# Kernel tuning notes

Hardware: AMD Instinct MI355X
Metric: run time of the kernel (lower is better)

Reference implementation:

```python
import jax, jax.numpy as jnp
import numpy as np

LOW_T = 0.3
HIGH_T = 0.7
H_IMG = 2048
W_IMG = 2048


def _any8(a, g):
    # OR over the 8 neighbors at offset +-g (the original connected() checks
    # the 8 compass neighbors at distance `gap`).
    H, W = a.shape
    p = jnp.pad(a, g)
    def s(dy, dx):
        return p[g + dy:g + dy + H, g + dx:g + dx + W]
    return (s(-g, -g) | s(-g, 0) | s(-g, g)
            | s(0, -g) | s(0, g)
            | s(g, -g) | s(g, 0) | s(g, g))


def _bound_mask(H, W, g):
    # original boundary rule: x-g >= 0, y-g >= 0, x+g < W-1, y+g < H-1
    y = jnp.arange(H)[:, None]
    x = jnp.arange(W)[None, :]
    return (x >= g) & (y >= g) & (x + g < W - 1) & (y + g < H - 1)


def _hysteresis_active(lt2, hi2):
    # Fixed point of the flood-fill: weak pixels (low>0) become active when
    # 8-connected (gap 1 or 2) to an active pixel. Parallel conditional
    # dilation iterated to convergence.
    H, W = lt2.shape
    tmask = _bound_mask(H, W, 1)   # trace() in-bounds condition
    c1 = _bound_mask(H, W, 1)
    c2 = _bound_mask(H, W, 2)
    weak = lt2 > 0.0

    def cond(state):
        return state[1]

    def body(state):
        active, _ = state
        conn = (c1 & _any8(active, 1)) | (c2 & _any8(active, 2))
        new = active | (tmask & weak & conn)
        return new, jnp.any(new != active)

    active0 = hi2 > 0.0
    active, _ = jax.lax.while_loop(cond, body, (active0, jnp.array(True)))
    return active


def setup_inputs() -> dict:
    key = jax.random.key(0)
    k1, k2, k3 = jax.random.split(key, 3)
    shape = (1, 1, H_IMG, W_IMG)
    return {
        "thin_edges": jax.random.uniform(k1, shape, jnp.float32),
        "grad_magnitude": jax.random.normal(k2, shape, jnp.float32),
        "grad_orientation": jax.random.normal(k3, shape, jnp.float32),
    }


def reference(thin_edges, grad_magnitude, grad_orientation):
    low_thresholded = jnp.where(thin_edges < LOW_T, 0.0, thin_edges)
    high_threshold = jnp.where(thin_edges < HIGH_T, 0.0, thin_edges)
    lt2 = low_thresholded[0, 0]
    hi2 = high_threshold[0, 0]
    active = _hysteresis_active(lt2, hi2)
    # strong pixels keep their (high) value; promoted weak pixels take low value
    final2 = jnp.where(hi2 > 0.0, hi2, jnp.where(active, lt2, 0.0))
    final_thresholded = final2[None, None]
    return (low_thresholded, high_threshold, final_thresholded)
```

## Files before the change

### kernel.cpp

```cpp
#include <hip/hip_runtime.h>
#include <cstdint>

typedef unsigned long long u64;
typedef unsigned char u8;

#define H_IMG 2048
#define W_IMG 2048
#define WPR   32
#define NWORDS (H_IMG * WPR)
#define NPIX  (H_IMG * W_IMG)

#define TILE_H    8
#define HALO      32
#define PH        (TILE_H + 2 * HALO)
#define RS        33
#define RPG       (PH / 8)
#define MAX_PASS  64

__global__ __launch_bounds__(256) void init_kernel(const float4* __restrict__ thin4,
                                                   u8* __restrict__ wk8,
                                                   u8* __restrict__ st8) {
    int t  = blockIdx.x * 256 + threadIdx.x;
    int f0 = t * 2;
    float4 v0 = thin4[f0];
    float4 v1 = thin4[f0 + 1];
    unsigned wm = 0, sm = 0;

    wm |= ((v0.x >= 0.3f) ? 1u : 0u) << 0;
    wm |= ((v0.y >= 0.3f) ? 1u : 0u) << 1;
    wm |= ((v0.z >= 0.3f) ? 1u : 0u) << 2;
    wm |= ((v0.w >= 0.3f) ? 1u : 0u) << 3;
    sm |= ((v0.x >= 0.7f) ? 1u : 0u) << 0;
    sm |= ((v0.y >= 0.7f) ? 1u : 0u) << 1;
    sm |= ((v0.z >= 0.7f) ? 1u : 0u) << 2;
    sm |= ((v0.w >= 0.7f) ? 1u : 0u) << 3;

    wm |= ((v1.x >= 0.3f) ? 1u : 0u) << 4;
    wm |= ((v1.y >= 0.3f) ? 1u : 0u) << 5;
    wm |= ((v1.z >= 0.3f) ? 1u : 0u) << 6;
    wm |= ((v1.w >= 0.3f) ? 1u : 0u) << 7;
    sm |= ((v1.x >= 0.7f) ? 1u : 0u) << 4;
    sm |= ((v1.y >= 0.7f) ? 1u : 0u) << 5;
    sm |= ((v1.z >= 0.7f) ? 1u : 0u) << 6;
    sm |= ((v1.w >= 0.7f) ? 1u : 0u) << 7;

    wk8[t] = (u8)wm;
    st8[t] = (u8)sm;
}

__global__ __launch_bounds__(256) void flood_final(const u64* __restrict__ act,
                                                   const u64* __restrict__ weak,
                                                   const float4* __restrict__ thin4,
                                                   float4* __restrict__ lo4,
                                                   float4* __restrict__ hi4,
                                                   float4* __restrict__ out4) {
    __shared__ u64 buf[PH * RS];
    __shared__ u8 fA[PH], fB[PH];
    __shared__ int chg[3];

    const int tid = threadIdx.x;
    const int c   = tid & 31;
    const int tg  = tid >> 5;
    const int r0  = tg * RPG;
    const int rowBase = (int)blockIdx.x * TILE_H - HALO;

    u64 wreg[RPG], m1r[RPG], m2r[RPG];
    #pragma unroll
    for (int k = 0; k < RPG; ++k) {
        int lr = r0 + k;
        int gy = rowBase + lr;
        u64 a = 0, w = 0;
        if ((unsigned)gy < (unsigned)H_IMG) {
            a = act[gy * WPR + c];
            w = weak[gy * WPR + c];
        }
        buf[lr * RS + c] = a;
        wreg[k] = w;
        u64 m1 = (gy >= 1 && gy + 1 < H_IMG - 1) ? ~0ull : 0ull;
        u64 m2 = (gy >= 2 && gy + 2 < H_IMG - 1) ? ~0ull : 0ull;
        if (c == 0)       { m1 &= ~1ull;         m2 &= ~3ull; }
        if (c == WPR - 1) { m1 &= ~(3ull << 62); m2 &= ~(7ull << 61); }
        m1r[k] = m1;
        m2r[k] = m2;
    }
    if (c < RPG) fA[r0 + c] = 1;
    if (tid == 0) chg[0] = 0;
    u8* prevF = fA;
    u8* curF  = fB;
    __syncthreads();

    for (int pass = 0; pass < MAX_PASS; ++pass) {
        if (tid == 0) chg[(pass + 1) % 3] = 0;
        if (c < RPG) curF[r0 + c] = 0;

        int rj = r0 - 2 + c;
        u8  f  = (c < 13 && (unsigned)rj < (unsigned)PH) ? prevF[rj] : (u8)0;
        u64 bal = __ballot(f != 0);
        unsigned Hm = ((unsigned)bal | (unsigned)(bal >> 32)) & 0x1fffu;
        int myc = 0;

        if (Hm) {
            int i0  = __builtin_ctz(Hm);
            int i1  = 31 - __builtin_clz(Hm);
            int klo = (i0 > 4) ? (i0 - 4) : 0;
            int khi = (i1 < RPG - 1) ? i1 : (RPG - 1);

            u64 cc[5], s1[5], s2[5];

            #define LOAD_ROW(slot, LR, COND) do {                                    \
                int _lr = (LR);                                                      \
                u64 _C = 0, _L = 0, _R = 0;                                          \
                if ((COND) && (unsigned)_lr < (unsigned)PH) {                        \
                    _C = buf[_lr * RS + c];                                          \
                    if (c > 0)       _L = buf[_lr * RS + c - 1];                     \
                    if (c < WPR - 1) _R = buf[_lr * RS + c + 1];                     \
                }                                                                    \
                cc[slot] = _C;                                                       \
                s1[slot] = ((_C << 1) | (_L >> 63)) | ((_C >> 1) | (_R << 63));      \
                s2[slot] = ((_C << 2) | (_L >> 62)) | ((_C >> 2) | (_R << 62));      \
            } while (0)

            LOAD_ROW(0, r0 - 2, (klo <= 0));
            LOAD_ROW(1, r0 - 1, (klo <= 1));
            LOAD_ROW(2, r0 + 0, (klo <= 2));
            LOAD_ROW(3, r0 + 1, (klo <= 3));

            #pragma unroll
            for (int k = 0; k < RPG; ++k) {
                LOAD_ROW(4, r0 + k + 2, (k >= klo - 4 && k <= khi));
                if (k >= klo && k <= khi) {
                    u64 a1 = (s1[1] | cc[1]) | (s1[3] | cc[3]) | s1[2];
                    u64 a2 = (s2[0] | cc[0]) | (s2[4] | cc[4]) | s2[2];
                    u64 nv = cc[2] | (wreg[k] & ((m1r[k] & a1) | (m2r[k] & a2)));
                    int ch = (nv != cc[2]);
                    u64 b2 = __ballot(ch);
                    if (ch) buf[(r0 + k) * RS + c] = nv;
                    unsigned hm = (unsigned)(b2 >> (tid & 32));
                    if (c == 0 && hm) curF[r0 + k] = 1;
                    myc |= ch;
                }
                cc[0] = cc[1]; cc[1] = cc[2]; cc[2] = cc[3]; cc[3] = cc[4];
                s1[0] = s1[1]; s1[1] = s1[2]; s1[2] = s1[3]; s1[3] = s1[4];
                s2[0] = s2[1]; s2[1] = s2[2]; s2[2] = s2[3]; s2[3] = s2[4];
            }
            #undef LOAD_ROW
        }

        if (myc) chg[pass % 3] = 1;
        __syncthreads();
        if (chg[pass % 3] == 0) break;
        u8* t = prevF; prevF = curF; curF = t;
    }

    const int B = blockIdx.x;
    #pragma unroll
    for (int j = 0; j < 16; ++j) {
        int f   = tid + 256 * j;
        int px  = f * 4;
        int r   = px >> 11;
        int col = px & 2047;
        u64 w   = buf[(HALO + r) * RS + (col >> 6)];
        int b   = col & 63;
        float4 v = thin4[B * 4096 + f];
        float4 lo, hi, o;
        lo.x = (v.x < 0.3f) ? 0.0f : v.x;  hi.x = (v.x < 0.7f) ? 0.0f : v.x;
        lo.y = (v.y < 0.3f) ? 0.0f : v.y;  hi.y = (v.y < 0.7f) ? 0.0f : v.y;
        lo.z = (v.z < 0.3f) ? 0.0f : v.z;  hi.z = (v.z < 0.7f) ? 0.0f : v.z;
        lo.w = (v.w < 0.3f) ? 0.0f : v.w;  hi.w = (v.w < 0.7f) ? 0.0f : v.w;
        o.x = ((w >> (b + 0)) & 1ull) ? lo.x : 0.0f;
        o.y = ((w >> (b + 1)) & 1ull) ? lo.y : 0.0f;
        o.z = ((w >> (b + 2)) & 1ull) ? lo.z : 0.0f;
        o.w = ((w >> (b + 3)) & 1ull) ? lo.w : 0.0f;
        lo4 [B * 4096 + f] = lo;
        hi4 [B * 4096 + f] = hi;
        out4[B * 4096 + f] = o;
    }
}

extern "C" void kernel_launch(void* const* d_in, const int* in_sizes, int n_in,
                              void* d_out, int out_size, void* d_ws, size_t ws_size,
                              hipStream_t stream) {
    const float* thin = (const float*)d_in[0];
    float* out_low   = (float*)d_out;
    float* out_high  = out_low + NPIX;
    float* out_final = out_high + NPIX;

    u8* wk8 = (u8*)d_ws;
    u8* st8 = wk8 + NWORDS * 8;

    init_kernel<<<NPIX / (8 * 256), 256, 0, stream>>>(
        (const float4*)thin, wk8, st8);

    flood_final<<<H_IMG / TILE_H, 256, 0, stream>>>(
        (const u64*)st8, (const u64*)wk8, (const float4*)thin,
        (float4*)out_low, (float4*)out_high, (float4*)out_final);
}
```

Before: 108.6 us.

## Write threshold outputs in init kernel and only zero unreached weak pixels after flood

The init kernel now writes the low, high and a provisional final output (the low-thresholded value) straight from the input values it already loads. The flood kernel no longer rereads the input or rewrites full rows. It only scatters zeros into the final output for weak pixels that did not become active. This moves the dense output traffic into the simple streaming kernel and leaves the flood kernel with a sparse store tail. The cost is scattered 4-byte stores, whose number depends on how many weak pixels stay unreached.

```diff
diff --git a/kernel.cpp b/kernel.cpp
--- a/kernel.cpp
+++ b/kernel.cpp
@@ -19,7 +19,10 @@
 
 __global__ __launch_bounds__(256) void init_kernel(const float4* __restrict__ thin4,
                                                    u8* __restrict__ wk8,
-                                                   u8* __restrict__ st8) {
+                                                   u8* __restrict__ st8,
+                                                   float4* __restrict__ lo4,
+                                                   float4* __restrict__ hi4,
+                                                   float4* __restrict__ out4) {
     int t  = blockIdx.x * 256 + threadIdx.x;
     int f0 = t * 2;
     float4 v0 = thin4[f0];
@@ -46,14 +49,28 @@
 
     wk8[t] = (u8)wm;
     st8[t] = (u8)sm;
+
+    float4 l0, h0, l1, h1;
+    l0.x = (v0.x < 0.3f) ? 0.0f : v0.x;  h0.x = (v0.x < 0.7f) ? 0.0f : v0.x;
+    l0.y = (v0.y < 0.3f) ? 0.0f : v0.y;  h0.y = (v0.y < 0.7f) ? 0.0f : v0.y;
+    l0.z = (v0.z < 0.3f) ? 0.0f : v0.z;  h0.z = (v0.z < 0.7f) ? 0.0f : v0.z;
+    l0.w = (v0.w < 0.3f) ? 0.0f : v0.w;  h0.w = (v0.w < 0.7f) ? 0.0f : v0.w;
+    l1.x = (v1.x < 0.3f) ? 0.0f : v1.x;  h1.x = (v1.x < 0.7f) ? 0.0f : v1.x;
+    l1.y = (v1.y < 0.3f) ? 0.0f : v1.y;  h1.y = (v1.y < 0.7f) ? 0.0f : v1.y;
+    l1.z = (v1.z < 0.3f) ? 0.0f : v1.z;  h1.z = (v1.z < 0.7f) ? 0.0f : v1.z;
+    l1.w = (v1.w < 0.3f) ? 0.0f : v1.w;  h1.w = (v1.w < 0.7f) ? 0.0f : v1.w;
+
+    lo4 [f0]     = l0;
+    lo4 [f0 + 1] = l1;
+    hi4 [f0]     = h0;
+    hi4 [f0 + 1] = h1;
+    out4[f0]     = l0;
+    out4[f0 + 1] = l1;
 }
 
 __global__ __launch_bounds__(256) void flood_final(const u64* __restrict__ act,
                                                    const u64* __restrict__ weak,
-                                                   const float4* __restrict__ thin4,
-                                                   float4* __restrict__ lo4,
-                                                   float4* __restrict__ hi4,
-                                                   float4* __restrict__ out4) {
+                                                   float* __restrict__ out) {
     __shared__ u64 buf[PH * RS];
     __shared__ u8 fA[PH], fB[PH];
     __shared__ int chg[3];
@@ -152,28 +169,18 @@
         u8* t = prevF; prevF = curF; curF = t;
     }
 
-    const int B = blockIdx.x;
-    #pragma unroll
-    for (int j = 0; j < 16; ++j) {
-        int f   = tid + 256 * j;
-        int px  = f * 4;
-        int r   = px >> 11;
-        int col = px & 2047;
-        u64 w   = buf[(HALO + r) * RS + (col >> 6)];
-        int b   = col & 63;
-        float4 v = thin4[B * 4096 + f];
-        float4 lo, hi, o;
-        lo.x = (v.x < 0.3f) ? 0.0f : v.x;  hi.x = (v.x < 0.7f) ? 0.0f : v.x;
-        lo.y = (v.y < 0.3f) ? 0.0f : v.y;  hi.y = (v.y < 0.7f) ? 0.0f : v.y;
-        lo.z = (v.z < 0.3f) ? 0.0f : v.z;  hi.z = (v.z < 0.7f) ? 0.0f : v.z;
-        lo.w = (v.w < 0.3f) ? 0.0f : v.w;  hi.w = (v.w < 0.7f) ? 0.0f : v.w;
-        o.x = ((w >> (b + 0)) & 1ull) ? lo.x : 0.0f;
-        o.y = ((w >> (b + 1)) & 1ull) ? lo.y : 0.0f;
-        o.z = ((w >> (b + 2)) & 1ull) ? lo.z : 0.0f;
-        o.w = ((w >> (b + 3)) & 1ull) ? lo.w : 0.0f;
-        lo4 [B * 4096 + f] = lo;
-        hi4 [B * 4096 + f] = hi;
-        out4[B * 4096 + f] = o;
+    {
+        const int B  = blockIdx.x;
+        int gy = B * TILE_H + tg;
+        u64 a  = buf[(HALO + tg) * RS + c];
+        u64 w  = weak[gy * WPR + c];
+        u64 z  = w & ~a;
+        float* orow = out + (size_t)gy * W_IMG + (c << 6);
+        while (z) {
+            int b = __builtin_ctzll(z);
+            z &= z - 1;
+            orow[b] = 0.0f;
+        }
     }
 }
 
@@ -189,9 +196,9 @@
     u8* st8 = wk8 + NWORDS * 8;
 
     init_kernel<<<NPIX / (8 * 256), 256, 0, stream>>>(
-        (const float4*)thin, wk8, st8);
+        (const float4*)thin, wk8, st8,
+        (float4*)out_low, (float4*)out_high, (float4*)out_final);
 
     flood_final<<<H_IMG / TILE_H, 256, 0, stream>>>(
-        (const u64*)st8, (const u64*)wk8, (const float4*)thin,
-        (float4*)out_low, (float4*)out_high, (float4*)out_final);
+        (const u64*)st8, (const u64*)wk8, out_final);
 }
```

Result: no change. 110.1 us (+1.5%).
